# Performance work log

Measured on AMD Instinct MI355X. Metric: run time of the kernel, lower is better.

The kernel has to match this reference:

```python
import jax, jax.numpy as jnp
import numpy as np

NUM_HEADS = 16
HEAD_DIM = 64
D_MODEL = NUM_HEADS * HEAD_DIM
EPS = 1e-8
SCALE = 1.0 / np.sqrt(HEAD_DIM)


def setup_inputs() -> dict:
    key = jax.random.key(0)
    ks = jax.random.split(key, 5)
    B, S = 2, 2048
    w_std = 1.0 / np.sqrt(D_MODEL)
    return {
        "x": jax.random.normal(ks[0], (B, S, D_MODEL), dtype=jnp.float32),
        "Wq": jax.random.normal(ks[1], (D_MODEL, D_MODEL), dtype=jnp.float32) * w_std,
        "Wk": jax.random.normal(ks[2], (D_MODEL, D_MODEL), dtype=jnp.float32) * w_std,
        "Wv": jax.random.normal(ks[3], (D_MODEL, D_MODEL), dtype=jnp.float32) * w_std,
        "Wo": jax.random.normal(ks[4], (D_MODEL, D_MODEL), dtype=jnp.float32) * w_std,
        "xsa_scale": jnp.ones((1,), dtype=jnp.float32),
    }


def reference(x, Wq, Wk, Wv, Wo, xsa_scale):
    B, S, _ = x.shape
    # torch nn.Linear(no bias): y = x @ W.T
    def proj(W):
        y = jnp.einsum("bsd,ed->bse", x, W)
        # (B, S, D) -> (B, H, S, Dh)
        return y.reshape(B, S, NUM_HEADS, HEAD_DIM).transpose(0, 2, 1, 3)

    q, k, v = proj(Wq), proj(Wk), proj(Wv)
    scores = jnp.einsum("bhqd,bhkd->bhqk", q, k) * SCALE
    attn = jax.nn.softmax(scores, axis=-1)
    out = jnp.einsum("bhqk,bhkd->bhqd", attn, v)
    # subtract_projection: remove component of out along each token's own v
    dot = jnp.sum(out * v, axis=-1, keepdims=True)
    v_norm_sq = jnp.sum(v * v, axis=-1, keepdims=True) + EPS
    out = out - xsa_scale * (dot / v_norm_sq) * v
    out = out.transpose(0, 2, 1, 3).reshape(B, S, D_MODEL)
    return jnp.einsum("bsd,ed->bse", out, Wo)


if __name__ == "__main__":
    print(reference(**setup_inputs()).shape)
```

## Files before the change

### kernel.cpp

```cpp
#include <hip/hip_runtime.h>
#include <math.h>

#define BATCH 2
#define SEQ   2048
#define NH    16
#define HD    64
#define DM    1024
#define MROWS (BATCH * SEQ)
#define NEL   ((size_t)MROWS * DM)
#define WEL   ((size_t)DM * DM)
#define SM_SCALE_LOG2E 0.18033688011112042f

typedef __bf16 bf16x8 __attribute__((ext_vector_type(8)));
typedef float  f32x4  __attribute__((ext_vector_type(4)));

#define MFMA16(a, b, c) __builtin_amdgcn_mfma_f32_16x16x32_bf16((a), (b), (c), 0, 0, 0)
#define EXP2(x) __builtin_amdgcn_exp2f(x)

#define GLDS16(g, s) __builtin_amdgcn_global_load_lds( \
    (const __attribute__((address_space(1))) void*)(g), \
    (__attribute__((address_space(3))) void*)(s), 16, 0, 0)


__global__ __launch_bounds__(256) void cvt_all(
    const float* __restrict__ x,
    const float* __restrict__ w0, const float* __restrict__ w1,
    const float* __restrict__ w2, const float* __restrict__ w3,
    __bf16* __restrict__ xb, __bf16* __restrict__ wb)
{
    const int bid = blockIdx.x;
    const float* src;
    __bf16* dst;
    size_t base;
    if (bid < 4096) {
        src = x; dst = xb; base = (size_t)bid * 1024;
    } else {
        const int r = bid - 4096;
        const int z = r >> 10;
        src = (z == 0) ? w0 : (z == 1) ? w1 : (z == 2) ? w2 : w3;
        dst = wb + (size_t)z * WEL;
        base = (size_t)(r & 1023) * 1024;
    }
    const size_t i = base + (size_t)threadIdx.x * 4;
    const float4 f = *(const float4*)&src[i];
    __bf16 b[4] = {(__bf16)f.x, (__bf16)f.y, (__bf16)f.z, (__bf16)f.w};
    *(ushort4*)&dst[i] = *(ushort4*)b;
}

template<int BN, int NZ>
__global__ __launch_bounds__(256) void gemm_nt_mfma(
    const __bf16* __restrict__ A, const __bf16* __restrict__ W0,
    void* __restrict__ C0, __bf16* __restrict__ Vt, int mode)
{
    constexpr int NI  = BN / 32;
    constexpr int NIT = DM / 32;
    constexpr int NX  = DM / BN;
    constexpr int LNX = (BN == 128) ? 3 : 4;
    __shared__ __bf16 lds[2 * 128 * 32 + 2 * BN * 32];
    #define AST(buf) (lds + (buf) * 4096)
    #define BST(buf) (lds + 8192 + (buf) * (BN * 32))

    const int t = threadIdx.x;
    const int w = t >> 6, l = t & 63;
    const int quad = l >> 4, l15 = l & 15;

    const int id  = blockIdx.x;
    const int xcd = id & 7;
    const int g   = id >> 3;
    const int x   = g & (NX - 1);
    const int r0  = g >> LNX;
    const int z   = r0 >> 2;
    const int yq  = r0 & 3;
    const int y   = xcd * 4 + yq;
    const int m0 = y * 128, n0 = x * BN;
    const int wm = (w >> 1) * 64, wn = (w & 1) * (BN / 2);

    const __bf16* Wp = W0 + (size_t)z * WEL;

    const int lrow = l >> 2;
    const int lkof = ((l & 3) ^ ((lrow >> 1) & 3)) * 8;
    const int qsw = (quad ^ ((l15 >> 1) & 3)) * 8;

    const __bf16* Ag = A + (size_t)(m0 + w * 32 + lrow) * DM + lkof;
    const int aoff = (w * 32) * 32;
    const int brow = (BN == 128) ? (w * 32) : (w * 16);
    const __bf16* Bg = Wp + (size_t)(n0 + brow + lrow) * DM + lkof;
    const int boff = brow * 32;

    f32x4 acc[4][NI];
    #pragma unroll
    for (int i = 0; i < 4; i++)
        #pragma unroll
        for (int j = 0; j < NI; j++) acc[i][j] = (f32x4)0.0f;

    GLDS16(Ag,           AST(0) + aoff);
    GLDS16(Ag + 16 * DM, AST(0) + aoff + 512);
    GLDS16(Bg,           BST(0) + boff);
    if (BN == 128) GLDS16(Bg + 16 * DM, BST(0) + boff + 512);
    __syncthreads();

    for (int i = 0; i < NIT; i++) {
        const int cur = i & 1, nxt = cur ^ 1;
        if (i + 1 < NIT) {
            const int k0 = (i + 1) * 32;
            GLDS16(Ag + k0,           AST(nxt) + aoff);
            GLDS16(Ag + k0 + 16 * DM, AST(nxt) + aoff + 512);
            GLDS16(Bg + k0,           BST(nxt) + boff);
            if (BN == 128) GLDS16(Bg + k0 + 16 * DM, BST(nxt) + boff + 512);
        }

        bf16x8 af[4], bfr[NI];
        #pragma unroll
        for (int mi = 0; mi < 4; mi++)
            af[mi] = *(const bf16x8*)&AST(cur)[(wm + mi * 16 + l15) * 32 + qsw];
        #pragma unroll
        for (int ni = 0; ni < NI; ni++)
            bfr[ni] = *(const bf16x8*)&BST(cur)[(wn + ni * 16 + l15) * 32 + qsw];
        __builtin_amdgcn_s_setprio(1);
        #pragma unroll
        for (int mi = 0; mi < 4; mi++)
            #pragma unroll
            for (int ni = 0; ni < NI; ni++)
                acc[mi][ni] = MFMA16(af[mi], bfr[ni], acc[mi][ni]);
        __builtin_amdgcn_s_setprio(0);

        __syncthreads();
    }

    if (mode) {
        const float sc = (z == 0) ? SM_SCALE_LOG2E : 1.0f;
        __bf16* C = (__bf16*)C0 + (size_t)z * NEL;
        #pragma unroll
        for (int mi = 0; mi < 4; mi++)
            #pragma unroll
            for (int ni = 0; ni < NI; ni++)
                #pragma unroll
                for (int r = 0; r < 4; r++) {
                    const int row = m0 + wm + mi * 16 + quad * 4 + r;
                    const int col = n0 + wn + ni * 16 + l15;
                    const int b = row >> 11, s = row & (SEQ - 1);
                    const int h = col >> 6,  d = col & (HD - 1);
                    const __bf16 val = (__bf16)(acc[mi][ni][r] * sc);
                    C[((size_t)(b * NH + h) * SEQ + s) * HD + d] = val;
                }

        if constexpr (BN == 128) {
            if (z == 2) {
                __bf16* T = lds;
                #pragma unroll
                for (int mi = 0; mi < 4; mi++)
                    #pragma unroll
                    for (int ni = 0; ni < 4; ni++) {
                        const int cl = wn + ni * 16 + l15;
                        const int s0 = wm + mi * 16 + quad * 4;
                        __bf16 pb[4] = {(__bf16)acc[mi][ni][0], (__bf16)acc[mi][ni][1],
                                        (__bf16)acc[mi][ni][2], (__bf16)acc[mi][ni][3]};
                        const int scn = s0 >> 3;
                        const int sub = (s0 >> 2) & 1;
                        *(uint2*)&T[cl * 128 + ((scn ^ (cl & 7)) * 8) + sub * 4] =
                            *(uint2*)pb;
                    }
                __syncthreads();
                const int b = m0 >> 11;
                const int sbase = m0 & (SEQ - 1);
                #pragma unroll
                for (int u = 0; u < 8; u++) {
                    const int cl = ((u >> 1) * 32) + (t >> 3);
                    const int ci = (u & 1) * 8 + (t & 7);
                    const int hh = (n0 + cl) >> 6, dd = (n0 + cl) & (HD - 1);
                    const uint4 v = *(const uint4*)&T[cl * 128 + ((ci ^ (cl & 7)) * 8)];
                    *(uint4*)&Vt[((size_t)(b * NH + hh) * HD + dd) * SEQ +
                                 sbase + ci * 8] = v;
                }
            }
        }
    } else {
        float* C = (float*)C0;
        #pragma unroll
        for (int mi = 0; mi < 4; mi++)
            #pragma unroll
            for (int ni = 0; ni < NI; ni++)
                #pragma unroll
                for (int r = 0; r < 4; r++) {
                    const int row = m0 + wm + mi * 16 + quad * 4 + r;
                    const int col = n0 + wn + ni * 16 + l15;
                    C[(size_t)row * DM + col] = acc[mi][ni][r];
                }
    }
    #undef AST
    #undef BST
}

__global__ __launch_bounds__(512, 2) void attn_mfma(
    const __bf16* __restrict__ Q, const __bf16* __restrict__ K,
    const __bf16* __restrict__ Vt, const __bf16* __restrict__ V,
    const float* __restrict__ xsa, __bf16* __restrict__ X2)
{
    __shared__ __bf16 KV[2][2][8192];
    __shared__ __bf16 Pt[8][32][64];

    const int t = threadIdx.x;
    const int w = t >> 6, l = t & 63;
    const int quad = l >> 4, l15 = l & 15;
    const int bh = blockIdx.x & 31;
    const int q0 = (blockIdx.x >> 5) * 256;

    const __bf16* Qb  = Q  + (size_t)bh * SEQ * HD;
    const __bf16* Kb  = K  + (size_t)bh * SEQ * HD;
    const __bf16* Vtb = Vt + (size_t)bh * HD * SEQ;

    const int lrow = l >> 2;
    const int lkof = ((l & 3) ^ ((lrow >> 1) & 3)) * 8;
    const int qsw = (quad ^ ((l15 >> 1) & 3)) * 8;
    const int pkey = l15 & 7;

    const int vkg = w >> 1;
    const int vr0 = (w & 1) * 32;

    __bf16* Qst = &KV[1][0][0];
    #pragma unroll
    for (int h = 0; h < 2; h++)
        #pragma unroll
        for (int qq = 0; qq < 2; qq++)
            GLDS16(Qb + (size_t)(q0 + w * 32 + qq * 16 + lrow) * HD + h * 32 + lkof,
                   Qst + h * 8192 + (w * 32 + qq * 16) * 32);
    #pragma unroll
    for (int h = 0; h < 2; h++)
        GLDS16(Kb + (size_t)(w * 16 + lrow) * HD + h * 32 + lkof,
               &KV[0][0][h * 4096 + (w * 16) * 32]);
    #pragma unroll
    for (int qq = 0; qq < 2; qq++)
        GLDS16(Vtb + (size_t)(vr0 + qq * 16 + lrow) * SEQ + vkg * 32 + lkof,
               &KV[0][1][vkg * 2048 + (vr0 + qq * 16) * 32]);
    __syncthreads();

    bf16x8 qf[2][2];
    #pragma unroll
    for (int h = 0; h < 2; h++)
        #pragma unroll
        for (int mi = 0; mi < 2; mi++)
            qf[h][mi] = *(const bf16x8*)&Qst[h * 8192 +
                          (w * 32 + mi * 16 + l15) * 32 + qsw];
    __syncthreads();

    float l_i[2] = {0.0f, 0.0f};
    f32x4 o[2][4];
    #pragma unroll
    for (int mi = 0; mi < 2; mi++)
        #pragma unroll
        for (int db = 0; db < 4; db++) o[mi][db] = (f32x4)0.0f;

    constexpr int NT = SEQ / 128;
    for (int kt = 0; kt < NT; kt++) {
        const int cur = kt & 1, nxt = cur ^ 1;
        if (kt + 1 < NT) {
            const int k0n = (kt + 1) * 128;
            #pragma unroll
            for (int h = 0; h < 2; h++)
                GLDS16(Kb + (size_t)(k0n + w * 16 + lrow) * HD + h * 32 + lkof,
                       &KV[nxt][0][h * 4096 + (w * 16) * 32]);
            #pragma unroll
            for (int qq = 0; qq < 2; qq++)
                GLDS16(Vtb + (size_t)(vr0 + qq * 16 + lrow) * SEQ + k0n + vkg * 32 + lkof,
                       &KV[nxt][1][vkg * 2048 + (vr0 + qq * 16) * 32]);
        }
        const __bf16* Ks = &KV[cur][0][0];
        const __bf16* Vs = &KV[cur][1][0];

        #pragma unroll
        for (int sub = 0; sub < 2; sub++) {
            f32x4 st[2][4];
            #pragma unroll
            for (int mi = 0; mi < 2; mi++)
                #pragma unroll
                for (int kb = 0; kb < 4; kb++) st[mi][kb] = (f32x4)0.0f;
            __builtin_amdgcn_s_setprio(1);
            #pragma unroll
            for (int h = 0; h < 2; h++)
                #pragma unroll
                for (int kb = 0; kb < 4; kb++) {
                    const bf16x8 kf = *(const bf16x8*)&Ks[h * 4096 +
                                          (sub * 64 + kb * 16 + l15) * 32 + qsw];
                    #pragma unroll
                    for (int mi = 0; mi < 2; mi++)
                        st[mi][kb] = MFMA16(kf, qf[h][mi], st[mi][kb]);
                }
            __builtin_amdgcn_s_setprio(0);

            #pragma unroll
            for (int mi = 0; mi < 2; mi++) {
                float rs = 0.0f;
                #pragma unroll
                for (int kb = 0; kb < 4; kb++)
                    #pragma unroll
                    for (int r = 0; r < 4; r++) {
                        const float p = EXP2(st[mi][kb][r]);
                        st[mi][kb][r] = p;
                        rs += p;
                    }
                l_i[mi] += rs;
                #pragma unroll
                for (int kb = 0; kb < 4; kb++) {
                    __bf16 pb[4] = {(__bf16)st[mi][kb][0], (__bf16)st[mi][kb][1],
                                    (__bf16)st[mi][kb][2], (__bf16)st[mi][kb][3]};
                    const int pc = ((kb * 2 + (quad >> 1)) ^ pkey) * 8 + (quad & 1) * 4;
                    *(uint2*)&Pt[w][mi * 16 + l15][pc] = *(uint2*)pb;
                }
            }

            #pragma unroll
            for (int kh = 0; kh < 2; kh++) {
                bf16x8 pf[2];
                #pragma unroll
                for (int mi = 0; mi < 2; mi++) {
                    const int pc = ((kh * 4 + quad) ^ pkey) * 8;
                    pf[mi] = *(const bf16x8*)&Pt[w][mi * 16 + l15][pc];
                }
                __builtin_amdgcn_s_setprio(1);
                #pragma unroll
                for (int db = 0; db < 4; db++) {
                    const bf16x8 vf = *(const bf16x8*)&Vs[(sub * 2 + kh) * 2048 +
                                          (db * 16 + l15) * 32 + qsw];
                    #pragma unroll
                    for (int mi = 0; mi < 2; mi++)
                        o[mi][db] = MFMA16(vf, pf[mi], o[mi][db]);
                }
                __builtin_amdgcn_s_setprio(0);
            }
        }

        __syncthreads();
    }

    const float xs = xsa[0];
    const int b = bh >> 4, h = bh & (NH - 1);
    const __bf16* Vb = V + (size_t)bh * SEQ * HD;
    #pragma unroll
    for (int mi = 0; mi < 2; mi++) {
        l_i[mi] += __shfl_xor(l_i[mi], 16);
        l_i[mi] += __shfl_xor(l_i[mi], 32);
        const int q = q0 + w * 32 + mi * 16 + l15;
        const float inv = 1.0f / l_i[mi];
        float vv[4][4], on[4][4];
        float dp = 0.0f, nn = 0.0f;
        #pragma unroll
        for (int db = 0; db < 4; db++) {
            __bf16 vb4[4];
            *(uint2*)vb4 = *(const uint2*)&Vb[(size_t)q * HD + db * 16 + quad * 4];
            #pragma unroll
            for (int r = 0; r < 4; r++) {
                const float vf = (float)vb4[r];
                const float of = o[mi][db][r] * inv;
                vv[db][r] = vf;
                on[db][r] = of;
                dp += of * vf;
                nn += vf * vf;
            }
        }
        dp += __shfl_xor(dp, 16); dp += __shfl_xor(dp, 32);
        nn += __shfl_xor(nn, 16); nn += __shfl_xor(nn, 32);
        const float coef = xs * dp / (nn + 1e-8f);
        #pragma unroll
        for (int db = 0; db < 4; db++) {
            __bf16 ob[4];
            #pragma unroll
            for (int r = 0; r < 4; r++)
                ob[r] = (__bf16)(on[db][r] - coef * vv[db][r]);
            *(uint2*)&X2[((size_t)b * SEQ + q) * DM + h * HD + db * 16 + quad * 4] =
                *(uint2*)ob;
        }
    }
}

extern "C" void kernel_launch(void* const* d_in, const int* in_sizes, int n_in,
                              void* d_out, int out_size, void* d_ws, size_t ws_size,
                              hipStream_t stream)
{
    (void)in_sizes; (void)n_in; (void)out_size; (void)ws_size;
    const float* x   = (const float*)d_in[0];
    const float* Wq  = (const float*)d_in[1];
    const float* Wk  = (const float*)d_in[2];
    const float* Wv  = (const float*)d_in[3];
    const float* Wo  = (const float*)d_in[4];
    const float* xsa = (const float*)d_in[5];
    float* out = (float*)d_out;

    __bf16* xb  = (__bf16*)d_ws;
    __bf16* Wb  = xb  + NEL;
    __bf16* Qb  = Wb  + 4 * WEL;
    __bf16* Kb  = Qb  + NEL;
    __bf16* Vb  = Kb  + NEL;
    __bf16* Vtb = Vb  + NEL;
    __bf16* X2  = Vtb + NEL;

    cvt_all<<<dim3(8192), 256, 0, stream>>>(x, Wq, Wk, Wv, Wo, xb, Wb);

    gemm_nt_mfma<128, 3><<<dim3(768), 256, 0, stream>>>(
        xb, Wb, Qb, Vtb, 1);

    attn_mfma<<<dim3((SEQ / 256) * BATCH * NH), 512, 0, stream>>>(
        Qb, Kb, Vtb, Vb, xsa, X2);

    gemm_nt_mfma<128, 1><<<dim3(256), 256, 0, stream>>>(
        X2, Wb + 3 * WEL, out, nullptr, 0);
}
```

Measured before the change: 183.2 us.

## Halve attention query tile per block and shrink output GEMM tile for occupancy

The attention kernel now handles 128 queries per block, with each wave owning 16 query rows instead of 32, and launches twice as many blocks. Its launch bounds are raised to 4 blocks per CU and the P staging buffer is halved. The output projection switches to a 64-wide N tile with 512 blocks, the QKV GEMM gets a min-blocks hint, and the attention output buffer reuses the x-bf16 workspace. The aim is more blocks in flight and better CU fill on the 256-CU part, at the cost of half the MFMA reuse of each K/V tile load per block and therefore more K/V traffic.

```diff
diff --git a/kernel.cpp b/kernel.cpp
--- a/kernel.cpp
+++ b/kernel.cpp
@@ -48,7 +48,7 @@
 }
 
 template<int BN, int NZ>
-__global__ __launch_bounds__(256) void gemm_nt_mfma(
+__global__ __launch_bounds__(256, 3) void gemm_nt_mfma(
     const __bf16* __restrict__ A, const __bf16* __restrict__ W0,
     void* __restrict__ C0, __bf16* __restrict__ Vt, int mode)
 {
@@ -191,19 +191,19 @@
     #undef BST
 }
 
-__global__ __launch_bounds__(512, 2) void attn_mfma(
+__global__ __launch_bounds__(512, 4) void attn_mfma(
     const __bf16* __restrict__ Q, const __bf16* __restrict__ K,
     const __bf16* __restrict__ Vt, const __bf16* __restrict__ V,
     const float* __restrict__ xsa, __bf16* __restrict__ X2)
 {
     __shared__ __bf16 KV[2][2][8192];
-    __shared__ __bf16 Pt[8][32][64];
+    __shared__ __bf16 Pt[8][16][64];
 
     const int t = threadIdx.x;
     const int w = t >> 6, l = t & 63;
     const int quad = l >> 4, l15 = l & 15;
     const int bh = blockIdx.x & 31;
-    const int q0 = (blockIdx.x >> 5) * 256;
+    const int q0 = (blockIdx.x >> 5) * 128;
 
     const __bf16* Qb  = Q  + (size_t)bh * SEQ * HD;
     const __bf16* Kb  = K  + (size_t)bh * SEQ * HD;
@@ -220,35 +220,28 @@
     __bf16* Qst = &KV[1][0][0];
     #pragma unroll
     for (int h = 0; h < 2; h++)
-        #pragma unroll
-        for (int qq = 0; qq < 2; qq++)
-            GLDS16(Qb + (size_t)(q0 + w * 32 + qq * 16 + lrow) * HD + h * 32 + lkof,
-                   Qst + h * 8192 + (w * 32 + qq * 16) * 32);
+        GLDS16(Qb + (size_t)(q0 + w * 16 + lrow) * HD + h * 32 + lkof,
+               Qst + h * 4096 + (w * 16) * 32);
     #pragma unroll
     for (int h = 0; h < 2; h++)
         GLDS16(Kb + (size_t)(w * 16 + lrow) * HD + h * 32 + lkof,
                &KV[0][0][h * 4096 + (w * 16) * 32]);
     #pragma unroll
-    for (int qq = 0; qq < 2; qq++)
-        GLDS16(Vtb + (size_t)(vr0 + qq * 16 + lrow) * SEQ + vkg * 32 + lkof,
-               &KV[0][1][vkg * 2048 + (vr0 + qq * 16) * 32]);
+    for (int u = 0; u < 2; u++)
+        GLDS16(Vtb + (size_t)(vr0 + u * 16 + lrow) * SEQ + vkg * 32 + lkof,
+               &KV[0][1][vkg * 2048 + (vr0 + u * 16) * 32]);
     __syncthreads();
 
-    bf16x8 qf[2][2];
+    bf16x8 qf[2];
     #pragma unroll
     for (int h = 0; h < 2; h++)
-        #pragma unroll
-        for (int mi = 0; mi < 2; mi++)
-            qf[h][mi] = *(const bf16x8*)&Qst[h * 8192 +
-                          (w * 32 + mi * 16 + l15) * 32 + qsw];
+        qf[h] = *(const bf16x8*)&Qst[h * 4096 + (w * 16 + l15) * 32 + qsw];
     __syncthreads();
 
-    float l_i[2] = {0.0f, 0.0f};
-    f32x4 o[2][4];
-    #pragma unroll
-    for (int mi = 0; mi < 2; mi++)
-        #pragma unroll
-        for (int db = 0; db < 4; db++) o[mi][db] = (f32x4)0.0f;
+    float l_i = 0.0f;
+    f32x4 o[4];
+    #pragma unroll
+    for (int db = 0; db < 4; db++) o[db] = (f32x4)0.0f;
 
     constexpr int NT = SEQ / 128;
     for (int kt = 0; kt < NT; kt++) {
@@ -260,20 +253,18 @@
                 GLDS16(Kb + (size_t)(k0n + w * 16 + lrow) * HD + h * 32 + lkof,
                        &KV[nxt][0][h * 4096 + (w * 16) * 32]);
             #pragma unroll
-            for (int qq = 0; qq < 2; qq++)
-                GLDS16(Vtb + (size_t)(vr0 + qq * 16 + lrow) * SEQ + k0n + vkg * 32 + lkof,
-                       &KV[nxt][1][vkg * 2048 + (vr0 + qq * 16) * 32]);
+            for (int u = 0; u < 2; u++)
+                GLDS16(Vtb + (size_t)(vr0 + u * 16 + lrow) * SEQ + k0n + vkg * 32 + lkof,
+                       &KV[nxt][1][vkg * 2048 + (vr0 + u * 16) * 32]);
         }
         const __bf16* Ks = &KV[cur][0][0];
         const __bf16* Vs = &KV[cur][1][0];
 
         #pragma unroll
         for (int sub = 0; sub < 2; sub++) {
-            f32x4 st[2][4];
-            #pragma unroll
-            for (int mi = 0; mi < 2; mi++)
-                #pragma unroll
-                for (int kb = 0; kb < 4; kb++) st[mi][kb] = (f32x4)0.0f;
+            f32x4 st[4];
+            #pragma unroll
+            for (int kb = 0; kb < 4; kb++) st[kb] = (f32x4)0.0f;
             __builtin_amdgcn_s_setprio(1);
             #pragma unroll
             for (int h = 0; h < 2; h++)
@@ -281,49 +272,40 @@
                 for (int kb = 0; kb < 4; kb++) {
                     const bf16x8 kf = *(const bf16x8*)&Ks[h * 4096 +
                                           (sub * 64 + kb * 16 + l15) * 32 + qsw];
-                    #pragma unroll
-                    for (int mi = 0; mi < 2; mi++)
-                        st[mi][kb] = MFMA16(kf, qf[h][mi], st[mi][kb]);
+                    st[kb] = MFMA16(kf, qf[h], st[kb]);
                 }
             __builtin_amdgcn_s_setprio(0);
 
-            #pragma unroll
-            for (int mi = 0; mi < 2; mi++) {
+            {
                 float rs = 0.0f;
                 #pragma unroll
                 for (int kb = 0; kb < 4; kb++)
                     #pragma unroll
                     for (int r = 0; r < 4; r++) {
-                        const float p = EXP2(st[mi][kb][r]);
-                        st[mi][kb][r] = p;
+                        const float p = EXP2(st[kb][r]);
+                        st[kb][r] = p;
                         rs += p;
                     }
-                l_i[mi] += rs;
+                l_i += rs;
                 #pragma unroll
                 for (int kb = 0; kb < 4; kb++) {
-                    __bf16 pb[4] = {(__bf16)st[mi][kb][0], (__bf16)st[mi][kb][1],
-                                    (__bf16)st[mi][kb][2], (__bf16)st[mi][kb][3]};
+                    __bf16 pb[4] = {(__bf16)st[kb][0], (__bf16)st[kb][1],
+                                    (__bf16)st[kb][2], (__bf16)st[kb][3]};
                     const int pc = ((kb * 2 + (quad >> 1)) ^ pkey) * 8 + (quad & 1) * 4;
-                    *(uint2*)&Pt[w][mi * 16 + l15][pc] = *(uint2*)pb;
+                    *(uint2*)&Pt[w][l15][pc] = *(uint2*)pb;
                 }
             }
 
             #pragma unroll
             for (int kh = 0; kh < 2; kh++) {
-                bf16x8 pf[2];
-                #pragma unroll
-                for (int mi = 0; mi < 2; mi++) {
-                    const int pc = ((kh * 4 + quad) ^ pkey) * 8;
-                    pf[mi] = *(const bf16x8*)&Pt[w][mi * 16 + l15][pc];
-                }
+                const int pc = ((kh * 4 + quad) ^ pkey) * 8;
+                const bf16x8 pf = *(const bf16x8*)&Pt[w][l15][pc];
                 __builtin_amdgcn_s_setprio(1);
                 #pragma unroll
                 for (int db = 0; db < 4; db++) {
                     const bf16x8 vf = *(const bf16x8*)&Vs[(sub * 2 + kh) * 2048 +
                                           (db * 16 + l15) * 32 + qsw];
-                    #pragma unroll
-                    for (int mi = 0; mi < 2; mi++)
-                        o[mi][db] = MFMA16(vf, pf[mi], o[mi][db]);
+                    o[db] = MFMA16(vf, pf, o[db]);
                 }
                 __builtin_amdgcn_s_setprio(0);
             }
@@ -335,12 +317,11 @@
     const float xs = xsa[0];
     const int b = bh >> 4, h = bh & (NH - 1);
     const __bf16* Vb = V + (size_t)bh * SEQ * HD;
-    #pragma unroll
-    for (int mi = 0; mi < 2; mi++) {
-        l_i[mi] += __shfl_xor(l_i[mi], 16);
-        l_i[mi] += __shfl_xor(l_i[mi], 32);
-        const int q = q0 + w * 32 + mi * 16 + l15;
-        const float inv = 1.0f / l_i[mi];
+    {
+        l_i += __shfl_xor(l_i, 16);
+        l_i += __shfl_xor(l_i, 32);
+        const int q = q0 + w * 16 + l15;
+        const float inv = 1.0f / l_i;
         float vv[4][4], on[4][4];
         float dp = 0.0f, nn = 0.0f;
         #pragma unroll
@@ -350,7 +331,7 @@
             #pragma unroll
             for (int r = 0; r < 4; r++) {
                 const float vf = (float)vb4[r];
-                const float of = o[mi][db][r] * inv;
+                const float of = o[db][r] * inv;
                 vv[db][r] = vf;
                 on[db][r] = of;
                 dp += of * vf;
@@ -391,16 +372,16 @@
     __bf16* Kb  = Qb  + NEL;
     __bf16* Vb  = Kb  + NEL;
     __bf16* Vtb = Vb  + NEL;
-    __bf16* X2  = Vtb + NEL;
+    __bf16* X2  = xb;
 
     cvt_all<<<dim3(8192), 256, 0, stream>>>(x, Wq, Wk, Wv, Wo, xb, Wb);
 
     gemm_nt_mfma<128, 3><<<dim3(768), 256, 0, stream>>>(
         xb, Wb, Qb, Vtb, 1);
 
-    attn_mfma<<<dim3((SEQ / 256) * BATCH * NH), 512, 0, stream>>>(
+    attn_mfma<<<dim3((SEQ / 128) * BATCH * NH), 512, 0, stream>>>(
         Qb, Kb, Vtb, Vb, xsa, X2);
 
-    gemm_nt_mfma<128, 1><<<dim3(256), 256, 0, stream>>>(
+    gemm_nt_mfma<64, 1><<<dim3(512), 256, 0, stream>>>(
         X2, Wb + 3 * WEL, out, nullptr, 0);
 }
```

Measured after the change: 178.4 us, median of 2. 2.6% less time.
